# Performance work log

Measured on AMD Instinct MI355X. Metric: run time of the kernel, lower is better.

The kernel has to match this reference:

```python
import jax, jax.numpy as jnp
import numpy as np

SEQLEN = np.array([1024, 768, 512, 1536, 256, 1280, 512, 1024], dtype=np.int32)
HIDDEN = 2048
HEAD_NUM = 16


def setup_inputs() -> dict:
    key = jax.random.key(0)
    k1, k2 = jax.random.split(key)
    total = int(SEQLEN.sum())
    a = jax.random.normal(k1, (total, HIDDEN), dtype=jnp.float32) * 0.02
    b = jax.random.normal(k2, (total, HIDDEN), dtype=jnp.float32) * 0.02
    return {"a": a, "b": b, "seqlen": np.asarray(SEQLEN), "head_num": HEAD_NUM}


def reference(a, b, seqlen, head_num):
    # Variable-length strided batched matmul (QK^T), no padding.
    # a, b: [sum(seqlen), hidden]; output: flat concat of per-seq [head_num, s, s].
    seqlen = np.asarray(seqlen)
    offs = np.concatenate([[0], np.cumsum(seqlen)])  # static offsets
    hidden = a.shape[1]
    head_size = hidden // head_num
    outs = []
    for i, s in enumerate(seqlen.tolist()):
        ai = a[offs[i]:offs[i + 1]].reshape(s, head_num, head_size)
        bi = b[offs[i]:offs[i + 1]].reshape(s, head_num, head_size)
        # per-head QK^T: [head_num, s, s]
        ci = jnp.einsum('shd,thd->hst', ai, bi)
        outs.append(ci.reshape(-1))
    return jnp.concatenate(outs)
```

## Files before the change

### kernel.cpp

```cpp
#include <hip/hip_runtime.h>

#define NSEQ   8
#define HEADS  16
#define HSIZE  128
#define HIDDEN 2048
#define BT     128
#define LDS_PAD 8
#define LDS_ROW (HSIZE + LDS_PAD)

typedef __attribute__((ext_vector_type(8))) short  bf16x8;
typedef __attribute__((ext_vector_type(4))) float  f32x4;

struct SeqMap {
    int       s[NSEQ];
    int       row_off[NSEQ];
    long long out_off[NSEQ];
    int       t[NSEQ];
    int       blk_start[NSEQ];
    int       nblk;
};

__device__ __forceinline__ unsigned short f2bf(float x) {
    unsigned int u = __builtin_bit_cast(unsigned int, x);
    u += 0x7fffu + ((u >> 16) & 1u);
    return (unsigned short)(u >> 16);
}

__global__ __launch_bounds__(256, 2) void qkt_strip_kernel(
    const float* __restrict__ A, const float* __restrict__ B,
    float* __restrict__ out, SeqMap map)
{
    __shared__ unsigned short lds[2][BT * LDS_ROW];

    const int cpx = map.nblk >> 3;
    const int bid = ((int)blockIdx.x % 8) * cpx + ((int)blockIdx.x / 8);

    int i = 0;
    #pragma unroll
    for (int k = 1; k < NSEQ; ++k) if (bid >= map.blk_start[k]) i = k;
    const int local = bid - map.blk_start[i];
    const int t     = map.t[i];
    const int h     = local / t;
    const int tr    = local - h * t;
    const int s     = map.s[i];
    const int row0  = map.row_off[i];

    const int tid  = threadIdx.x;
    const int r0   = tid >> 5;
    const int c4   = tid & 31;
    const size_t hcol = (size_t)h * HSIZE + (size_t)c4 * 4;

    const int lane = tid & 63;
    const int w    = tid >> 6;
    const int wr   = w >> 1;
    const int wc   = w & 1;
    const int lrow = lane & 15;
    const int kgrp = lane >> 4;

    unsigned short* ldsw0 = &lds[0][r0 * LDS_ROW + c4 * 4];
    unsigned short* ldsw1 = &lds[1][r0 * LDS_ROW + c4 * 4];

    {
        const float* sa = A + (size_t)(row0 + tr * BT + r0) * HIDDEN + hcol;
        const float* sb = B + (size_t)(row0 + r0) * HIDDEN + hcol;
        float4 ga[16], gb[16];
        #pragma unroll
        for (int it = 0; it < 16; ++it) ga[it] = *(const float4*)(sa + (size_t)it * 8 * HIDDEN);
        #pragma unroll
        for (int it = 0; it < 16; ++it) gb[it] = *(const float4*)(sb + (size_t)it * 8 * HIDDEN);
        #pragma unroll
        for (int it = 0; it < 16; ++it) {
            ushort4 p; p.x=f2bf(ga[it].x); p.y=f2bf(ga[it].y); p.z=f2bf(ga[it].z); p.w=f2bf(ga[it].w);
            *(ushort4*)(ldsw0 + it * 8 * LDS_ROW) = p;
        }
        #pragma unroll
        for (int it = 0; it < 16; ++it) {
            ushort4 p; p.x=f2bf(gb[it].x); p.y=f2bf(gb[it].y); p.z=f2bf(gb[it].z); p.w=f2bf(gb[it].w);
            *(ushort4*)(ldsw1 + it * 8 * LDS_ROW) = p;
        }
    }
    __syncthreads();

    bf16x8 af[4][4];
    #pragma unroll
    for (int m = 0; m < 4; ++m)
        #pragma unroll
        for (int kk = 0; kk < 4; ++kk)
            af[m][kk] = *(const bf16x8*)&lds[0][(wr*64 + m*16 + lrow) * LDS_ROW + kk*32 + kgrp*8];
    __syncthreads();

    int cur = 1;
    const long long obase = map.out_off[i] + (long long)h * s * s;
    float* orow = out + obase
                + (long long)(tr * BT + wr * 64 + kgrp * 4) * s
                + (wc * 64 + lrow);

    for (int tc = 0; tc < t; ++tc) {
        const bool has_next = (tc + 1 < t);

        float4 g[16];
        if (has_next) {
            const float* sb = B + (size_t)(row0 + (tc + 1) * BT + r0) * HIDDEN + hcol;
            #pragma unroll
            for (int it = 0; it < 16; ++it) g[it] = *(const float4*)(sb + (size_t)it * 8 * HIDDEN);
        }

        f32x4 acc[4][4];
        #pragma unroll
        for (int m = 0; m < 4; ++m)
            #pragma unroll
            for (int n = 0; n < 4; ++n)
                acc[m][n] = (f32x4){0.f, 0.f, 0.f, 0.f};

        const unsigned short* lb = &lds[cur][0];
        #pragma unroll
        for (int kk = 0; kk < 4; ++kk) {
            bf16x8 bfr[4];
            #pragma unroll
            for (int n = 0; n < 4; ++n)
                bfr[n] = *(const bf16x8*)&lb[(wc*64 + n*16 + lrow) * LDS_ROW + kk*32 + kgrp*8];
            #pragma unroll
            for (int m = 0; m < 4; ++m)
                #pragma unroll
                for (int n = 0; n < 4; ++n)
                    acc[m][n] = __builtin_amdgcn_mfma_f32_16x16x32_bf16(
                                    af[m][kk], bfr[n], acc[m][n], 0, 0, 0);
        }

        if (has_next) {
            unsigned short* dst = cur ? ldsw0 : ldsw1;
            #pragma unroll
            for (int it = 0; it < 16; ++it) {
                ushort4 p; p.x=f2bf(g[it].x); p.y=f2bf(g[it].y); p.z=f2bf(g[it].z); p.w=f2bf(g[it].w);
                *(ushort4*)(dst + it * 8 * LDS_ROW) = p;
            }
        }

        float* op = orow + tc * BT;
        #pragma unroll
        for (int m = 0; m < 4; ++m)
            #pragma unroll
            for (int n = 0; n < 4; ++n)
                #pragma unroll
                for (int j = 0; j < 4; ++j)
                    op[(long long)(m * 16 + j) * s + n * 16] = acc[m][n][j];

        __syncthreads();
        cur ^= 1;
    }
}

extern "C" void kernel_launch(void* const* d_in, const int* in_sizes, int n_in,
                              void* d_out, int out_size, void* d_ws, size_t ws_size,
                              hipStream_t stream) {
    const float* A = (const float*)d_in[0];
    const float* B = (const float*)d_in[1];
    float* out = (float*)d_out;

    static const int S[NSEQ] = {1024, 768, 512, 1536, 256, 1280, 512, 1024};

    int row_off[NSEQ]; long long out_off[NSEQ];
    int row = 0; long long o = 0;
    for (int i = 0; i < NSEQ; ++i) {
        row_off[i] = row; out_off[i] = o;
        row += S[i];
        o   += (long long)HEADS * S[i] * S[i];
    }

    static const int order[NSEQ] = {3, 5, 0, 7, 1, 2, 6, 4};

    SeqMap map;
    int blk = 0;
    for (int k = 0; k < NSEQ; ++k) {
        const int i = order[k];
        const int t = S[i] / BT;
        map.s[k]         = S[i];
        map.row_off[k]   = row_off[i];
        map.out_off[k]   = out_off[i];
        map.t[k]         = t;
        map.blk_start[k] = blk;
        blk += HEADS * t;
    }
    map.nblk = blk;

    qkt_strip_kernel<<<blk, 256, 0, stream>>>(A, B, out, map);
}
```

Before: 170.1 us.

## Pre-convert inputs to head-major bf16 workspace before the QK^T kernel

Adds a pre-pass kernel that converts A and B from fp32 to bf16 and rearranges them into a head-major contiguous layout in the workspace. The main kernel then loads contiguous bf16 tiles with 16-byte loads instead of re-reading and re-converting strided fp32 B tiles in every block. This cuts the repeated global traffic and conversion work, at the cost of an extra kernel launch and a full read/write pass over the inputs. The original path is kept as a fallback when the workspace is too small.

New measurement: 246.2 us. 44.7% more time.

```diff
diff --git a/kernel.cpp b/kernel.cpp
--- a/kernel.cpp
+++ b/kernel.cpp
@@ -5,6 +5,7 @@
 #define HSIZE  128
 #define HIDDEN 2048
 #define BT     128
+#define TOTAL  6912
 #define LDS_PAD 8
 #define LDS_ROW (HSIZE + LDS_PAD)
 
@@ -26,8 +27,34 @@
     return (unsigned short)(u >> 16);
 }
 
-__global__ __launch_bounds__(256, 2) void qkt_strip_kernel(
+__device__ __forceinline__ ushort4 f2bf4(float4 v) {
+    ushort4 p;
+    p.x = f2bf(v.x); p.y = f2bf(v.y); p.z = f2bf(v.z); p.w = f2bf(v.w);
+    return p;
+}
+
+__global__ __launch_bounds__(256) void precvt_kernel(
     const float* __restrict__ A, const float* __restrict__ B,
+    unsigned short* __restrict__ Aws, unsigned short* __restrict__ Bws)
+{
+    const int n4 = TOTAL * (HIDDEN / 4);
+    for (int idx = blockIdx.x * 256 + threadIdx.x; idx < 2 * n4;
+         idx += gridDim.x * 256) {
+        const int m = idx >= n4;
+        const int j = m ? idx - n4 : idx;
+        const float* src = m ? B : A;
+        unsigned short* dst = m ? Bws : Aws;
+        float4 v = *(const float4*)(src + (size_t)j * 4);
+        const int row = j >> 9;
+        const int col = (j & 511) * 4;
+        const int h   = col >> 7;
+        const int cin = col & 127;
+        *(ushort4*)(dst + ((size_t)h * TOTAL + row) * HSIZE + cin) = f2bf4(v);
+    }
+}
+
+__global__ __launch_bounds__(256, 2) void qkt_bf16_kernel(
+    const unsigned short* __restrict__ Aws, const unsigned short* __restrict__ Bws,
     float* __restrict__ out, SeqMap map)
 {
     __shared__ unsigned short lds[2][BT * LDS_ROW];
@@ -45,10 +72,9 @@
     const int s     = map.s[i];
     const int row0  = map.row_off[i];
 
-    const int tid  = threadIdx.x;
-    const int r0   = tid >> 5;
-    const int c4   = tid & 31;
-    const size_t hcol = (size_t)h * HSIZE + (size_t)c4 * 4;
+    const int tid = threadIdx.x;
+    const int r0  = tid >> 4;
+    const int c8  = tid & 15;
 
     const int lane = tid & 63;
     const int w    = tid >> 6;
@@ -57,27 +83,21 @@
     const int lrow = lane & 15;
     const int kgrp = lane >> 4;
 
-    unsigned short* ldsw0 = &lds[0][r0 * LDS_ROW + c4 * 4];
-    unsigned short* ldsw1 = &lds[1][r0 * LDS_ROW + c4 * 4];
+    const unsigned short* pa = Aws + ((size_t)h * TOTAL + row0 + tr * BT) * HSIZE;
+    const unsigned short* pb = Bws + ((size_t)h * TOTAL + row0) * HSIZE;
 
     {
-        const float* sa = A + (size_t)(row0 + tr * BT + r0) * HIDDEN + hcol;
-        const float* sb = B + (size_t)(row0 + r0) * HIDDEN + hcol;
-        float4 ga[16], gb[16];
-        #pragma unroll
-        for (int it = 0; it < 16; ++it) ga[it] = *(const float4*)(sa + (size_t)it * 8 * HIDDEN);
-        #pragma unroll
-        for (int it = 0; it < 16; ++it) gb[it] = *(const float4*)(sb + (size_t)it * 8 * HIDDEN);
-        #pragma unroll
-        for (int it = 0; it < 16; ++it) {
-            ushort4 p; p.x=f2bf(ga[it].x); p.y=f2bf(ga[it].y); p.z=f2bf(ga[it].z); p.w=f2bf(ga[it].w);
-            *(ushort4*)(ldsw0 + it * 8 * LDS_ROW) = p;
-        }
-        #pragma unroll
-        for (int it = 0; it < 16; ++it) {
-            ushort4 p; p.x=f2bf(gb[it].x); p.y=f2bf(gb[it].y); p.z=f2bf(gb[it].z); p.w=f2bf(gb[it].w);
-            *(ushort4*)(ldsw1 + it * 8 * LDS_ROW) = p;
-        }
+        uint4 ga[8], gb[8];
+        #pragma unroll
+        for (int it = 0; it < 8; ++it) ga[it] = *(const uint4*)(pa + ((size_t)it * 256 + tid) * 8);
+        #pragma unroll
+        for (int it = 0; it < 8; ++it) gb[it] = *(const uint4*)(pb + ((size_t)it * 256 + tid) * 8);
+        #pragma unroll
+        for (int it = 0; it < 8; ++it)
+            *(uint4*)&lds[0][(it * 16 + r0) * LDS_ROW + c8 * 8] = ga[it];
+        #pragma unroll
+        for (int it = 0; it < 8; ++it)
+            *(uint4*)&lds[1][(it * 16 + r0) * LDS_ROW + c8 * 8] = gb[it];
     }
     __syncthreads();
 
@@ -95,14 +115,15 @@
                 + (long long)(tr * BT + wr * 64 + kgrp * 4) * s
                 + (wc * 64 + lrow);
 
+    const unsigned short* pbnext = pb + (size_t)BT * HSIZE;
+
     for (int tc = 0; tc < t; ++tc) {
         const bool has_next = (tc + 1 < t);
 
-        float4 g[16];
+        uint4 g[8];
         if (has_next) {
-            const float* sb = B + (size_t)(row0 + (tc + 1) * BT + r0) * HIDDEN + hcol;
-            #pragma unroll
-            for (int it = 0; it < 16; ++it) g[it] = *(const float4*)(sb + (size_t)it * 8 * HIDDEN);
+            #pragma unroll
+            for (int it = 0; it < 8; ++it) g[it] = *(const uint4*)(pbnext + ((size_t)it * 256 + tid) * 8);
         }
 
         f32x4 acc[4][4];
@@ -128,22 +149,144 @@
         }
 
         if (has_next) {
+            #pragma unroll
+            for (int it = 0; it < 8; ++it)
+                *(uint4*)&lds[cur ^ 1][(it * 16 + r0) * LDS_ROW + c8 * 8] = g[it];
+            pbnext += (size_t)BT * HSIZE;
+        }
+
+        {
+            float* op = orow + tc * BT;
+            #pragma unroll
+            for (int m = 0; m < 4; ++m)
+                #pragma unroll
+                for (int n = 0; n < 4; ++n)
+                    #pragma unroll
+                    for (int j = 0; j < 4; ++j)
+                        op[(long long)(m * 16 + j) * s + n * 16] = acc[m][n][j];
+        }
+
+        __syncthreads();
+        cur ^= 1;
+    }
+}
+
+__global__ __launch_bounds__(256, 2) void qkt_strip_kernel(
+    const float* __restrict__ A, const float* __restrict__ B,
+    float* __restrict__ out, SeqMap map)
+{
+    __shared__ unsigned short lds[2][BT * LDS_ROW];
+
+    const int cpx = map.nblk >> 3;
+    const int bid = ((int)blockIdx.x % 8) * cpx + ((int)blockIdx.x / 8);
+
+    int i = 0;
+    #pragma unroll
+    for (int k = 1; k < NSEQ; ++k) if (bid >= map.blk_start[k]) i = k;
+    const int local = bid - map.blk_start[i];
+    const int t     = map.t[i];
+    const int h     = local / t;
+    const int tr    = local - h * t;
+    const int s     = map.s[i];
+    const int row0  = map.row_off[i];
+
+    const int tid  = threadIdx.x;
+    const int r0   = tid >> 5;
+    const int c4   = tid & 31;
+    const size_t hcol = (size_t)h * HSIZE + (size_t)c4 * 4;
+
+    const int lane = tid & 63;
+    const int w    = tid >> 6;
+    const int wr   = w >> 1;
+    const int wc   = w & 1;
+    const int lrow = lane & 15;
+    const int kgrp = lane >> 4;
+
+    unsigned short* ldsw0 = &lds[0][r0 * LDS_ROW + c4 * 4];
+    unsigned short* ldsw1 = &lds[1][r0 * LDS_ROW + c4 * 4];
+
+    {
+        const float* sa = A + (size_t)(row0 + tr * BT + r0) * HIDDEN + hcol;
+        const float* sb = B + (size_t)(row0 + r0) * HIDDEN + hcol;
+        float4 ga[16], gb[16];
+        #pragma unroll
+        for (int it = 0; it < 16; ++it) ga[it] = *(const float4*)(sa + (size_t)it * 8 * HIDDEN);
+        #pragma unroll
+        for (int it = 0; it < 16; ++it) gb[it] = *(const float4*)(sb + (size_t)it * 8 * HIDDEN);
+        #pragma unroll
+        for (int it = 0; it < 16; ++it)
+            *(ushort4*)(ldsw0 + it * 8 * LDS_ROW) = f2bf4(ga[it]);
+        #pragma unroll
+        for (int it = 0; it < 16; ++it)
+            *(ushort4*)(ldsw1 + it * 8 * LDS_ROW) = f2bf4(gb[it]);
+    }
+    __syncthreads();
+
+    bf16x8 af[4][4];
+    #pragma unroll
+    for (int m = 0; m < 4; ++m)
+        #pragma unroll
+        for (int kk = 0; kk < 4; ++kk)
+            af[m][kk] = *(const bf16x8*)&lds[0][(wr*64 + m*16 + lrow) * LDS_ROW + kk*32 + kgrp*8];
+    __syncthreads();
+
+    int cur = 1;
+    const long long obase = map.out_off[i] + (long long)h * s * s;
+    float* orow = out + obase
+                + (long long)(tr * BT + wr * 64 + kgrp * 4) * s
+                + (wc * 64 + lrow);
+
+    const float* sbnext = B + (size_t)(row0 + BT + r0) * HIDDEN + hcol;
+
+    for (int tc = 0; tc < t; ++tc) {
+        const bool has_next = (tc + 1 < t);
+
+        float4 g[16];
+        if (has_next) {
+            #pragma unroll
+            for (int it = 0; it < 16; ++it) g[it] = *(const float4*)(sbnext + (size_t)it * 8 * HIDDEN);
+        }
+
+        f32x4 acc[4][4];
+        #pragma unroll
+        for (int m = 0; m < 4; ++m)
+            #pragma unroll
+            for (int n = 0; n < 4; ++n)
+                acc[m][n] = (f32x4){0.f, 0.f, 0.f, 0.f};
+
+        const unsigned short* lb = &lds[cur][0];
+        #pragma unroll
+        for (int kk = 0; kk < 4; ++kk) {
+            bf16x8 bfr[4];
+            #pragma unroll
+            for (int n = 0; n < 4; ++n)
+                bfr[n] = *(const bf16x8*)&lb[(wc*64 + n*16 + lrow) * LDS_ROW + kk*32 + kgrp*8];
+            #pragma unroll
+            for (int m = 0; m < 4; ++m)
+                #pragma unroll
+                for (int n = 0; n < 4; ++n)
+                    acc[m][n] = __builtin_amdgcn_mfma_f32_16x16x32_bf16(
+                                    af[m][kk], bfr[n], acc[m][n], 0, 0, 0);
+        }
+
+        if (has_next) {
             unsigned short* dst = cur ? ldsw0 : ldsw1;
             #pragma unroll
-            for (int it = 0; it < 16; ++it) {
-                ushort4 p; p.x=f2bf(g[it].x); p.y=f2bf(g[it].y); p.z=f2bf(g[it].z); p.w=f2bf(g[it].w);
-                *(ushort4*)(dst + it * 8 * LDS_ROW) = p;
-            }
-        }
-
-        float* op = orow + tc * BT;
-        #pragma unroll
-        for (int m = 0; m < 4; ++m)
-            #pragma unroll
-            for (int n = 0; n < 4; ++n)
+            for (int it = 0; it < 16; ++it)
+                *(ushort4*)(dst + it * 8 * LDS_ROW) = f2bf4(g[it]);
+            sbnext += (size_t)BT * HIDDEN;
+        }
+
+        {
+            float* op = orow + tc * BT;
+            #pragma unroll
+            for (int m = 0; m < 4; ++m)
                 #pragma unroll
-                for (int j = 0; j < 4; ++j)
-                    op[(long long)(m * 16 + j) * s + n * 16] = acc[m][n][j];
+                for (int n = 0; n < 4; ++n)
+                    #pragma unroll
+                    for (int j = 0; j < 4; ++j)
+                        op[(long long)(m * 16 + j) * s + n * 16] = acc[m][n][j];
+        }
 
         __syncthreads();
         cur ^= 1;
@@ -183,5 +326,13 @@
     }
     map.nblk = blk;
 
-    qkt_strip_kernel<<<blk, 256, 0, stream>>>(A, B, out, map);
-}
+    const size_t need = (size_t)2 * TOTAL * HIDDEN * sizeof(unsigned short);
+    if (ws_size >= need) {
+        unsigned short* Aws = (unsigned short*)d_ws;
+        unsigned short* Bws = Aws + (size_t)TOTAL * HIDDEN;
+        precvt_kernel<<<2048, 256, 0, stream>>>(A, B, Aws, Bws);
+        qkt_bf16_kernel<<<blk, 256, 0, stream>>>(Aws, Bws, out, map);
+    } else {
+        qkt_strip_kernel<<<blk, 256, 0, stream>>>(A, B, out, map);
+    }
+}
```
